# Kernel tuning notes

Hardware: AMD Instinct MI355X
Metric: run time of the kernel (lower is better)

The kernel has to match this reference:

```python
import jax, jax.numpy as jnp
import numpy as np

B, S, D = 4, 2048, 2048          # batch, seq_len, num_hiddens (= query/key/value size)
H = 16                           # num_heads
DH = D // H                      # head dim = shared K/V projection dim


def setup_inputs() -> dict:
    key = jax.random.key(0)
    ks = jax.random.split(key, 11)
    s_in = 1.0 / np.sqrt(D)
    return {
        "q": jax.random.normal(ks[0], (B, S, D), jnp.float32),
        "k": jax.random.normal(ks[1], (B, S, D), jnp.float32),
        "v": jax.random.normal(ks[2], (B, S, D), jnp.float32),
        "Wq": jax.random.normal(ks[3], (D, D), jnp.float32) * s_in,
        "bq": jnp.zeros((D,), jnp.float32),
        "Wk": jax.random.normal(ks[4], (D, DH), jnp.float32) * s_in,
        "bk": jnp.zeros((DH,), jnp.float32),
        "Wv": jax.random.normal(ks[5], (D, DH), jnp.float32) * s_in,
        "bv": jnp.zeros((DH,), jnp.float32),
        "Wo": jax.random.normal(ks[6], (D, D), jnp.float32) * s_in,
        "bo": jnp.zeros((D,), jnp.float32),
    }


def reference(q, k, v, Wq, bq, Wk, bk, Wv, bv, Wo, bo):
    # Projections
    qh = (q @ Wq + bq).reshape(B, S, H, DH).transpose(0, 2, 1, 3)  # [B,H,S,DH]
    kh = k @ Wk + bk                                               # [B,S,DH] shared K head
    vh = v @ Wv + bv                                               # [B,S,DH] shared V head
    # Scaled dot-product attention with broadcast-shared K/V (no copies)
    scores = jnp.einsum('bhqd,bkd->bhqk', qh, kh) / jnp.sqrt(jnp.float32(DH))
    attn = jax.nn.softmax(scores, axis=-1)                          # [B,H,S,S]
    out = jnp.einsum('bhqk,bkd->bhqd', attn, vh)                    # [B,H,S,DH]
    out = out.transpose(0, 2, 1, 3).reshape(B, S, D)                # merge heads
    return out @ Wo + bo
```

## Files before the change

kernel.cpp:

```cpp
#include <hip/hip_runtime.h>
#include <stdint.h>

#define B_  4
#define S_  2048
#define D_  2048
#define H_  16
#define DH_ 128
#define M_  (B_*S_)

typedef unsigned short u16;
typedef __bf16 bf16x8 __attribute__((ext_vector_type(8)));
typedef float  f32x4  __attribute__((ext_vector_type(4)));
typedef u16    u16x4  __attribute__((ext_vector_type(4)));

__device__ __forceinline__ u16 f2bf(float f){
  unsigned x = __float_as_uint(f);
  x += 0x7fffu + ((x >> 16) & 1u);
  return (u16)(x >> 16);
}

__device__ __forceinline__ unsigned pkbf(float lo, float hi){
  unsigned r;
  asm("v_cvt_pk_bf16_f32 %0, %1, %2" : "=v"(r) : "v"(lo), "v"(hi));
  return r;
}

__device__ __forceinline__ void stage16(const void* g, void* lds_base){
  __builtin_amdgcn_global_load_lds(
      (const __attribute__((address_space(1))) void*)g,
      (__attribute__((address_space(3))) void*)lds_base, 16, 0, 0);
}

__device__ __forceinline__ f32x4 mfma16(bf16x8 a, bf16x8 b, f32x4 c){
  return __builtin_amdgcn_mfma_f32_16x16x32_bf16(a, b, c, 0, 0, 0);
}

__global__ void cvt_bf16(const float* __restrict__ s, u16* __restrict__ d, int n4){
  int i = blockIdx.x * 256 + threadIdx.x;
  if (i >= n4) return;
  float4 f = ((const float4*)s)[i];
  u16x4 u = { f2bf(f.x), f2bf(f.y), f2bf(f.z), f2bf(f.w) };
  ((u16x4*)d)[i] = u;
}

__global__ void transpose_bf(const float* __restrict__ W, u16* __restrict__ WT, int K, int N){
  __shared__ float tl[32][33];
  int n0 = blockIdx.x * 32, k0 = blockIdx.y * 32;
  int tx = threadIdx.x, ty = threadIdx.y;
  for (int r = 0; r < 4; r++)
    tl[ty + 8*r][tx] = W[(size_t)(k0 + ty + 8*r) * N + n0 + tx];
  __syncthreads();
  for (int r = 0; r < 4; r++)
    WT[(size_t)(n0 + ty + 8*r) * K + k0 + tx] = f2bf(tl[tx][ty + 8*r]);
}

__global__ void transpose_vh(const u16* __restrict__ vh, u16* __restrict__ vhT){
  __shared__ u16 tl[32][33];
  int b = blockIdx.z, d0 = blockIdx.x * 32, s0 = blockIdx.y * 32;
  int tx = threadIdx.x, ty = threadIdx.y;
  for (int r = 0; r < 4; r++)
    tl[ty + 8*r][tx] = vh[(size_t)(b * S_ + s0 + ty + 8*r) * DH_ + d0 + tx];
  __syncthreads();
  for (int r = 0; r < 4; r++)
    vhT[(size_t)(b * DH_ + d0 + ty + 8*r) * S_ + s0 + tx] = tl[tx][ty + 8*r];
}

template<int OUTF32>
__global__ __launch_bounds__(256) void gemm_bt(const u16* __restrict__ A,
    const u16* __restrict__ BT, const float* __restrict__ bias, void* __restrict__ Cv,
    int M, int N, int K)
{
  (void)M;
  __shared__ alignas(16) u16 Al[128 * 32];
  __shared__ alignas(16) u16 Bl[128 * 32];
  const int t = threadIdx.x, lane = t & 63, wave = t >> 6;
  const int quad = lane >> 4, lcol = lane & 15;
  const int m0 = blockIdx.y * 128, n0 = blockIdx.x * 128;
  const int wm = (wave >> 1) * 64, wn = (wave & 1) * 64;
  f32x4 acc[4][4] = {};
  for (int k0 = 0; k0 < K; k0 += 32) {
    for (int p = 0; p < 2; p++) {
      int c = p * 256 + wave * 64 + lane;
      int row = c >> 2, kc = c & 3;
      stage16(A  + (size_t)(m0 + row) * K + k0 + kc * 8, Al + (p*256 + wave*64) * 8);
      stage16(BT + (size_t)(n0 + row) * K + k0 + kc * 8, Bl + (p*256 + wave*64) * 8);
    }
    __syncthreads();
    bf16x8 af[4], bfr[4];
    for (int i = 0; i < 4; i++)
      af[i]  = *(const bf16x8*)(Al + (wm + i*16 + lcol) * 32 + quad * 8);
    for (int j = 0; j < 4; j++)
      bfr[j] = *(const bf16x8*)(Bl + (wn + j*16 + lcol) * 32 + quad * 8);
    for (int i = 0; i < 4; i++)
      for (int j = 0; j < 4; j++)
        acc[i][j] = mfma16(af[i], bfr[j], acc[i][j]);
    __syncthreads();
  }
  for (int j = 0; j < 4; j++) {
    int n = n0 + wn + j * 16 + lcol;
    float bj = bias[n];
    for (int i = 0; i < 4; i++) {
      int mbase = m0 + wm + i * 16 + quad * 4;
      for (int r = 0; r < 4; r++) {
        float vv = acc[i][j][r] + bj;
        if (OUTF32) ((float*)Cv)[(size_t)(mbase + r) * N + n] = vv;
        else        ((u16*)Cv)  [(size_t)(mbase + r) * N + n] = f2bf(vv);
      }
    }
  }
}

__global__ __launch_bounds__(256, 3) void mqa_attn(const u16* __restrict__ qh,
    const u16* __restrict__ kh, const u16* __restrict__ vhT, u16* __restrict__ ao)
{
  __shared__ alignas(16) u16 Kl[2][32 * 128];
  __shared__ alignas(16) u16 Vl[2][128 * 32];
  const int t = threadIdx.x, lane = t & 63, wave = t >> 6;
  const int quad = lane >> 4, lcol = lane & 15;
  const int b = blockIdx.z, h = blockIdx.y;
  const int q0 = blockIdx.x * 128 + wave * 32;
  const float sc2 = 0.12751743f;

  bf16x8 qf[2][4];
  for (int m = 0; m < 2; m++) {
    const u16* qp = qh + (size_t)(b * S_ + q0 + m * 16 + lcol) * D_ + h * DH_ + quad * 8;
    for (int kk = 0; kk < 4; kk++) qf[m][kk] = *(const bf16x8*)(qp + kk * 32);
  }
  union { u16 u[8]; bf16x8 v; } one_u;
  for (int i = 0; i < 8; i++) one_u.u[i] = 0x3F80;
  const bf16x8 ones = one_u.v;

  f32x4 o[2][8] = {};
  f32x4 al[2] = {};
  const u16* kb = kh  + (size_t)b * S_ * DH_;
  const u16* vb = vhT + (size_t)b * DH_ * S_;

  auto stageKV = [&](int tt, int bi) {
    int kv0 = tt * 32;
    for (int p = 0; p < 2; p++) {
      int c = p * 256 + wave * 64 + lane;
      int row = c >> 4, st = c & 15;
      int kc = st ^ (row & 15);
      stage16(kb + (size_t)(kv0 + row) * DH_ + kc * 8, &Kl[bi][(p*256 + wave*64) * 8]);
    }
    for (int p = 0; p < 2; p++) {
      int c = p * 256 + wave * 64 + lane;
      int row = c >> 2, st = c & 3;
      int kc = st ^ (row & 3) ^ ((row >> 2) & 3);
      stage16(vb + (size_t)row * S_ + kv0 + kc * 8, &Vl[bi][(p*256 + wave*64) * 8]);
    }
  };

  stageKV(0, 0);
  for (int tt = 0; tt < S_ / 32; tt++) {
    const int bi = tt & 1;
    __syncthreads();
    if (tt < S_ / 32 - 1) stageKV(tt + 1, bi ^ 1);

    const u16* Kb = &Kl[bi][0];
    const u16* Vb = &Vl[bi][0];

    unsigned cc[2][4];
    for (int kvf = 0; kvf < 2; kvf++) {
      f32x4 s[2] = {};
      const u16* kp = Kb + (size_t)(kvf * 16 + lcol) * 128;
      __builtin_amdgcn_s_setprio(1);
      for (int kk = 0; kk < 4; kk++) {
        int swz = (kk * 4 + quad) ^ lcol;
        bf16x8 kfr = *(const bf16x8*)(kp + swz * 8);
        for (int m = 0; m < 2; m++)
          s[m] = mfma16(kfr, qf[m][kk], s[m]);
      }
      __builtin_amdgcn_s_setprio(0);
      for (int m = 0; m < 2; m++) {
        float e0 = exp2f(s[m][0] * sc2), e1 = exp2f(s[m][1] * sc2);
        float e2 = exp2f(s[m][2] * sc2), e3 = exp2f(s[m][3] * sc2);
        cc[m][kvf * 2 + 0] = pkbf(e0, e1);
        cc[m][kvf * 2 + 1] = pkbf(e2, e3);
      }
    }
    bf16x8 pa[2];
    for (int m = 0; m < 2; m++) {
      asm("v_permlane32_swap_b32 %0, %1" : "+v"(cc[m][0]), "+v"(cc[m][2]));
      asm("v_permlane16_swap_b32 %0, %1" : "+v"(cc[m][0]), "+v"(cc[m][2]));
      asm("v_permlane32_swap_b32 %0, %1" : "+v"(cc[m][1]), "+v"(cc[m][3]));
      asm("v_permlane16_swap_b32 %0, %1" : "+v"(cc[m][1]), "+v"(cc[m][3]));
      union { unsigned u[4]; bf16x8 v; } pu;
      pu.u[0] = cc[m][0];
      pu.u[1] = cc[m][1];
      pu.u[2] = cc[m][2];
      pu.u[3] = cc[m][3];
      pa[m] = pu.v;
    }

    __builtin_amdgcn_s_setprio(1);
    for (int g = 0; g < 8; g++) {
      int swz = quad ^ (lcol & 3) ^ ((lcol >> 2) & 3);
      bf16x8 vfr = *(const bf16x8*)(Vb + (size_t)(g * 16 + lcol) * 32 + swz * 8);
      for (int m = 0; m < 2; m++)
        o[m][g] = mfma16(pa[m], vfr, o[m][g]);
    }
    for (int m = 0; m < 2; m++)
      al[m] = mfma16(pa[m], ones, al[m]);
    __builtin_amdgcn_s_setprio(0);
  }

  for (int m = 0; m < 2; m++) {
    u16* op = ao + (size_t)(b * S_ + q0 + m * 16 + quad * 4) * D_ + h * DH_ + lcol;
    for (int r = 0; r < 4; r++) {
      float inv = 1.0f / al[m][r];
      for (int g = 0; g < 8; g++)
        op[(size_t)r * D_ + g * 16] = f2bf(o[m][g][r] * inv);
    }
  }
}

extern "C" void kernel_launch(void* const* d_in, const int* in_sizes, int n_in,
                              void* d_out, int out_size, void* d_ws, size_t ws_size,
                              hipStream_t stream)
{
  (void)in_sizes; (void)n_in; (void)out_size;
  const float* q  = (const float*)d_in[0];
  const float* k  = (const float*)d_in[1];
  const float* v  = (const float*)d_in[2];
  const float* Wq = (const float*)d_in[3];
  const float* bq = (const float*)d_in[4];
  const float* Wk = (const float*)d_in[5];
  const float* bk = (const float*)d_in[6];
  const float* Wv = (const float*)d_in[7];
  const float* bv = (const float*)d_in[8];
  const float* Wo = (const float*)d_in[9];
  const float* bo = (const float*)d_in[10];
  float* out = (float*)d_out;

  char* ws = (char*)d_ws;
  size_t off = 0;
  auto alloc = [&](size_t bytes) -> char* {
    char* p = ws + off; off += (bytes + 255) & ~(size_t)255; return p;
  };
  u16* xbf = (u16*)alloc((size_t)M_ * D_ * 2);
  u16* qh  = (u16*)alloc((size_t)M_ * D_ * 2);
  u16* kh  = (u16*)alloc((size_t)M_ * DH_ * 2);
  u16* vh  = (u16*)alloc((size_t)M_ * DH_ * 2);
  u16* vhT = (u16*)alloc((size_t)M_ * DH_ * 2);
  u16* WqT = (u16*)alloc((size_t)D_ * D_ * 2);
  u16* WkT = (u16*)alloc((size_t)DH_ * D_ * 2);
  u16* WvT = (u16*)alloc((size_t)DH_ * D_ * 2);
  u16* WoT = (u16*)alloc((size_t)D_ * D_ * 2);
  u16* ao  = xbf;

  if (off > ws_size) return;

  const int n4 = M_ * D_ / 4;

  transpose_bf<<<dim3(D_/32,  D_/32), dim3(32, 8), 0, stream>>>(Wq, WqT, D_, D_);
  transpose_bf<<<dim3(DH_/32, D_/32), dim3(32, 8), 0, stream>>>(Wk, WkT, D_, DH_);
  transpose_bf<<<dim3(DH_/32, D_/32), dim3(32, 8), 0, stream>>>(Wv, WvT, D_, DH_);
  transpose_bf<<<dim3(D_/32,  D_/32), dim3(32, 8), 0, stream>>>(Wo, WoT, D_, D_);

  cvt_bf16<<<dim3(n4 / 256), dim3(256), 0, stream>>>(k, xbf, n4);
  gemm_bt<0><<<dim3(DH_/128, M_/128), dim3(256), 0, stream>>>(xbf, WkT, bk, kh, M_, DH_, D_);
  cvt_bf16<<<dim3(n4 / 256), dim3(256), 0, stream>>>(v, xbf, n4);
  gemm_bt<0><<<dim3(DH_/128, M_/128), dim3(256), 0, stream>>>(xbf, WvT, bv, vh, M_, DH_, D_);
  transpose_vh<<<dim3(DH_/32, S_/32, B_), dim3(32, 8), 0, stream>>>(vh, vhT);
  cvt_bf16<<<dim3(n4 / 256), dim3(256), 0, stream>>>(q, xbf, n4);
  gemm_bt<0><<<dim3(D_/128,  M_/128), dim3(256), 0, stream>>>(xbf, WqT, bq, qh, M_, D_, D_);

  mqa_attn<<<dim3(S_/128, H_, B_), dim3(256), 0, stream>>>(qh, kh, vhT, ao);

  gemm_bt<1><<<dim3(D_/128, M_/128), dim3(256), 0, stream>>>(ao, WoT, bo, out, M_, D_, D_);
}
```

Baseline: 742.0 us.

## Batch K/V conversions and projections into single launches with smaller M tiles

Merges the two fp32-to-bf16 conversions for k and v into one two-slice launch, using the not-yet-written qh buffer as scratch for the second input. Replaces the two separate K and V projection GEMMs, which launched only 64 blocks each with 128x128 tiles, with a dedicated kernel using 32x128 tiles and a z-dimension selecting K or V, giving 512 blocks to fill the GPU. The smaller tile has less data reuse per block and no double buffering, and it relies on qh being free until the Q projection overwrites it.

```diff
diff --git a/kernel.cpp b/kernel.cpp
--- a/kernel.cpp
+++ b/kernel.cpp
@@ -36,6 +36,17 @@
 }
 
 __global__ void cvt_bf16(const float* __restrict__ s, u16* __restrict__ d, int n4){
+  int i = blockIdx.x * 256 + threadIdx.x;
+  if (i >= n4) return;
+  float4 f = ((const float4*)s)[i];
+  u16x4 u = { f2bf(f.x), f2bf(f.y), f2bf(f.z), f2bf(f.w) };
+  ((u16x4*)d)[i] = u;
+}
+
+__global__ void cvt_bf16_2(const float* __restrict__ s0, const float* __restrict__ s1,
+                           u16* __restrict__ d0, u16* __restrict__ d1, int n4){
+  const float* s = blockIdx.y ? s1 : s0;
+  u16*        d = blockIdx.y ? d1 : d0;
   int i = blockIdx.x * 256 + threadIdx.x;
   if (i >= n4) return;
   float4 f = ((const float4*)s)[i];
@@ -110,6 +121,63 @@
   }
 }
 
+__global__ __launch_bounds__(256) void gemm_kv(
+    const u16* __restrict__ A0, const u16* __restrict__ A1,
+    const u16* __restrict__ BT0, const u16* __restrict__ BT1,
+    const float* __restrict__ b0, const float* __restrict__ b1,
+    u16* __restrict__ C0, u16* __restrict__ C1)
+{
+  const int sel = blockIdx.z;
+  const u16* A  = sel ? A1 : A0;
+  const u16* BT = sel ? BT1 : BT0;
+  const float* bias = sel ? b1 : b0;
+  u16* C = sel ? C1 : C0;
+
+  __shared__ alignas(16) u16 Al[32 * 32];
+  __shared__ alignas(16) u16 Bl[128 * 32];
+  const int t = threadIdx.x, lane = t & 63, wave = t >> 6;
+  const int quad = lane >> 4, lcol = lane & 15;
+  const int m0 = blockIdx.x * 32;
+
+  f32x4 acc[2][2] = {};
+  for (int k0 = 0; k0 < D_; k0 += 32) {
+    if (t < 128) {
+      int row = t >> 2, kc = t & 3;
+      stage16(A + (size_t)(m0 + row) * D_ + k0 + kc * 8, Al + (wave * 64) * 8);
+    } else {
+      int bc = t - 128, row = bc >> 2, kc = bc & 3;
+      stage16(BT + (size_t)row * D_ + k0 + kc * 8, Bl + ((wave - 2) * 64) * 8);
+    }
+    {
+      int bc = t + 128, row = bc >> 2, kc = bc & 3;
+      stage16(BT + (size_t)row * D_ + k0 + kc * 8, Bl + (128 + wave * 64) * 8);
+    }
+    if (t < 128) {
+      int bc = t + 384, row = bc >> 2, kc = bc & 3;
+      stage16(BT + (size_t)row * D_ + k0 + kc * 8, Bl + (384 + wave * 64) * 8);
+    }
+    __syncthreads();
+    bf16x8 af[2], bfr[2];
+    for (int i = 0; i < 2; i++)
+      af[i]  = *(const bf16x8*)(Al + (i*16 + lcol) * 32 + quad * 8);
+    for (int j = 0; j < 2; j++)
+      bfr[j] = *(const bf16x8*)(Bl + (wave*32 + j*16 + lcol) * 32 + quad * 8);
+    for (int i = 0; i < 2; i++)
+      for (int j = 0; j < 2; j++)
+        acc[i][j] = mfma16(af[i], bfr[j], acc[i][j]);
+    __syncthreads();
+  }
+  for (int j = 0; j < 2; j++) {
+    int n = wave * 32 + j * 16 + lcol;
+    float bj = bias[n];
+    for (int i = 0; i < 2; i++) {
+      int mbase = m0 + i * 16 + quad * 4;
+      for (int r = 0; r < 4; r++)
+        C[(size_t)(mbase + r) * DH_ + n] = f2bf(acc[i][j][r] + bj);
+    }
+  }
+}
+
 __global__ __launch_bounds__(256, 3) void mqa_attn(const u16* __restrict__ qh,
     const u16* __restrict__ kh, const u16* __restrict__ vhT, u16* __restrict__ ao)
 {
@@ -258,10 +326,9 @@
   transpose_bf<<<dim3(DH_/32, D_/32), dim3(32, 8), 0, stream>>>(Wv, WvT, D_, DH_);
   transpose_bf<<<dim3(D_/32,  D_/32), dim3(32, 8), 0, stream>>>(Wo, WoT, D_, D_);
 
-  cvt_bf16<<<dim3(n4 / 256), dim3(256), 0, stream>>>(k, xbf, n4);
-  gemm_bt<0><<<dim3(DH_/128, M_/128), dim3(256), 0, stream>>>(xbf, WkT, bk, kh, M_, DH_, D_);
-  cvt_bf16<<<dim3(n4 / 256), dim3(256), 0, stream>>>(v, xbf, n4);
-  gemm_bt<0><<<dim3(DH_/128, M_/128), dim3(256), 0, stream>>>(xbf, WvT, bv, vh, M_, DH_, D_);
+  cvt_bf16_2<<<dim3(n4 / 256, 2), dim3(256), 0, stream>>>(k, v, xbf, qh, n4);
+  gemm_kv<<<dim3(M_/32, 1, 2), dim3(256), 0, stream>>>(
+      xbf, qh, WkT, WvT, bk, bv, kh, vh);
   transpose_vh<<<dim3(DH_/32, S_/32, B_), dim3(32, 8), 0, stream>>>(vh, vhT);
   cvt_bf16<<<dim3(n4 / 256), dim3(256), 0, stream>>>(q, xbf, n4);
   gemm_bt<0><<<dim3(D_/128,  M_/128), dim3(256), 0, stream>>>(xbf, WqT, bq, qh, M_, D_, D_);
```

Result: faster. 684.5 us (-7.7%).
